# Performance work log

Hardware: AMD Instinct MI355X
Metric: run time of the kernel (lower is better)

The kernel has to match this reference:

```python
import math
import jax, jax.numpy as jnp
import numpy as np
from jax import lax

# ---- static config (mirrors RPN init + typical torchvision anchor setup) ----
IMG_H = IMG_W = 800
LEVELS = [(200, 200, 4, 32), (100, 100, 8, 64), (50, 50, 16, 128), (25, 25, 32, 256), (13, 13, 64, 512)]  # (h, w, stride, anchor_size)
RATIOS = (0.5, 1.0, 2.0)
COUNTS = tuple(h * w * len(RATIOS) for (h, w, _, _) in LEVELS)  # (120000,30000,7500,1875,507)
A_TOTAL = sum(COUNTS)  # 159882
PRE_NMS = 2000
POST_NMS = 1000
NMS_THRESH = 0.7
MIN_SIZE = 1e-3
BBOX_CLIP = math.log(1000.0 / 16)


def make_anchors():
    parts = []
    for (h, w, stride, size) in LEVELS:
        ws = np.array([size * np.sqrt(1.0 / r) for r in RATIOS], np.float32)  # [3]
        hs = np.array([size * np.sqrt(r) for r in RATIOS], np.float32)
        sx = (np.arange(w, dtype=np.float32) + 0.5) * stride
        sy = (np.arange(h, dtype=np.float32) + 0.5) * stride
        cy, cx = np.meshgrid(sy, sx, indexing='ij')
        cx = cx.reshape(-1, 1)
        cy = cy.reshape(-1, 1)
        a = np.stack([cx - ws / 2, cy - hs / 2, cx + ws / 2, cy + hs / 2], axis=-1)  # [HW,3,4]
        parts.append(a.reshape(-1, 4))
    return np.concatenate(parts, 0).astype(np.float32)


def setup_inputs() -> dict:
    key = jax.random.key(0)
    k1, k2 = jax.random.split(key)
    scores = jax.random.normal(k1, (1, A_TOTAL), dtype=jnp.float32)
    deltas = jax.random.normal(k2, (A_TOTAL, 4), dtype=jnp.float32) * 0.5
    anchors = jnp.asarray(make_anchors())
    return {'scores': scores, 'deltas': deltas, 'anchors': anchors}


def _pairwise_iou(b):
    area = (b[:, 2] - b[:, 0]) * (b[:, 3] - b[:, 1])  # [K]
    lt = jnp.maximum(b[:, None, :2], b[None, :, :2])   # [K,K,2]
    rb = jnp.minimum(b[:, None, 2:], b[None, :, 2:])
    wh = jnp.maximum(rb - lt, 0.0)
    inter = wh[..., 0] * wh[..., 1]
    return inter / (area[:, None] + area[None, :] - inter)


def reference(scores, deltas, anchors):
    s_all = lax.stop_gradient(scores[0])  # original does cls.detach()
    # ---- box decode (torchvision-style) ----
    w = anchors[:, 2] - anchors[:, 0]
    h = anchors[:, 3] - anchors[:, 1]
    cx = anchors[:, 0] + 0.5 * w
    cy = anchors[:, 1] + 0.5 * h
    dx, dy = deltas[:, 0], deltas[:, 1]
    dw = jnp.minimum(deltas[:, 2], BBOX_CLIP)
    dh = jnp.minimum(deltas[:, 3], BBOX_CLIP)
    px = cx + dx * w
    py = cy + dy * h
    pw = jnp.exp(dw) * w
    ph = jnp.exp(dh) * h
    boxes = jnp.stack([px - 0.5 * pw, py - 0.5 * ph, px + 0.5 * pw, py + 0.5 * ph], axis=1)  # [A,4]
    # ---- per-level top-k over objectness ----
    idx_parts = []
    off = 0
    for c in COUNTS:
        k = min(PRE_NMS, c)
        _, ti = lax.top_k(lax.dynamic_slice_in_dim(s_all, off, c), k)
        idx_parts.append(ti + off)
        off += c
    top_idx = jnp.concatenate(idx_parts)  # [K=8382]
    K = top_idx.shape[0]
    s = s_all[top_idx]
    b = boxes[top_idx]
    # ---- clip to image + min-size validity (masked instead of compacted) ----
    b = jnp.stack([jnp.clip(b[:, 0], 0.0, IMG_W), jnp.clip(b[:, 1], 0.0, IMG_H),
                   jnp.clip(b[:, 2], 0.0, IMG_W), jnp.clip(b[:, 3], 0.0, IMG_H)], axis=1)
    valid = ((b[:, 2] - b[:, 0]) >= MIN_SIZE) & ((b[:, 3] - b[:, 1]) >= MIN_SIZE)
    # ---- per-level NMS offset; replicates original feature_mask[keep] indexing
    # (positional indexing into the full anchor-order level-id vector) ----
    fmask_full = np.concatenate([np.full(c, i, np.float32) for i, c in enumerate(COUNTS)])
    fmask = jnp.asarray(fmask_full[:K])
    box_max = jnp.max(jnp.where(valid[:, None], b, -jnp.inf))
    bn = b + (fmask * (box_max + 1.0))[:, None]
    # ---- greedy NMS on score-sorted candidates ----
    s_m = jnp.where(valid, s, -jnp.inf)
    order = jnp.argsort(-s_m)
    s_srt = s_m[order]
    b_srt = b[order]
    iou = _pairwise_iou(bn[order])  # [K,K] ~281MB
    ar = jnp.arange(K)

    def body(i, keep):
        sup = (iou[i] > NMS_THRESH) & (ar > i)
        return jnp.where(keep[i], keep & ~sup, keep)

    keep = lax.fori_loop(0, K, body, s_srt > -jnp.inf)
    final = jnp.where(keep, s_srt, -jnp.inf)
    out_s, oidx = lax.top_k(final, POST_NMS)  # top post_nms kept, score order; -inf pads
    out_b = b_srt[oidx]
    return out_b, out_s
```

## Files before the change

kernel.cpp:

```cpp
#include <hip/hip_runtime.h>
#include <math.h>

typedef unsigned int u32;
typedef unsigned long long u64;
typedef unsigned char u8;

#define K_TOT 8382
#define NCH 131
#define CAP 1024
#define GCAP 32768
#define IMGSZ 800.0f

__device__ __constant__ int LOFF[5] = {0, 120000, 150000, 157500, 159375};
__device__ __constant__ int LCNT[5] = {120000, 30000, 7500, 1875, 507};
__device__ __constant__ int KSEL[5] = {2000, 2000, 2000, 1875, 507};
__device__ __constant__ int SELB[5] = {0, 2000, 4000, 6000, 7875};
__device__ __constant__ int HBS[4] = {0, 118, 148, 156};
__device__ __constant__ int GBS[6] = {0, 118, 148, 156, 158, 159};

static __device__ __forceinline__ u32 fkey(float x) {
    u32 u = __float_as_uint(x);
    u32 m = (u32)(((int)u) >> 31) | 0x80000000u;
    return u ^ m;
}

static __device__ __forceinline__ int lvl_of(int s) {
    return (s < 2000) ? 0 : (s < 4000) ? 1 : (s < 6000) ? 2 : (s < 7875) ? 3 : 4;
}

static __device__ __forceinline__ u32 rdl32(u32 v, int j) {
    return (u32)__builtin_amdgcn_readlane((int)v, j);
}
static __device__ __forceinline__ u64 rdlane64(u64 v, int j) {
    u32 lo = (u32)__builtin_amdgcn_readlane((int)(u32)v, j);
    u32 hi = (u32)__builtin_amdgcn_readlane((int)(u32)(v >> 32), j);
    return ((u64)hi << 32) | (u64)lo;
}

static __device__ __forceinline__ u32 wor32(u32 x) {
    x |= (u32)__builtin_amdgcn_update_dpp(0, (int)x, 0x111, 0xf, 0xf, true);
    x |= (u32)__builtin_amdgcn_update_dpp(0, (int)x, 0x112, 0xf, 0xf, true);
    x |= (u32)__builtin_amdgcn_update_dpp(0, (int)x, 0x114, 0xf, 0xf, true);
    x |= (u32)__builtin_amdgcn_update_dpp(0, (int)x, 0x118, 0xf, 0xf, true);
    x |= (u32)__builtin_amdgcn_update_dpp(0, (int)x, 0x142, 0xa, 0xf, true);
    x |= (u32)__builtin_amdgcn_update_dpp(0, (int)x, 0x143, 0xc, 0xf, true);
    return x;
}

static __device__ __forceinline__ void thresh_scan(const u32* hist, u32* scanbuf, int m,
                                                   u32 need, u32* sv, int t) {
    for (int i = t; i < m; i += 1024) scanbuf[i] = hist[m - 1 - i];
    __syncthreads();
    for (int ofs = 1; ofs < m; ofs <<= 1) {
        int i0 = t, i1 = t + 1024;
        u32 a0 = 0, a1 = 0;
        if (i0 < m && i0 >= ofs) a0 = scanbuf[i0 - ofs];
        if (i1 < m && i1 >= ofs) a1 = scanbuf[i1 - ofs];
        __syncthreads();
        if (i0 < m && i0 >= ofs) scanbuf[i0] += a0;
        if (i1 < m && i1 >= ofs) scanbuf[i1] += a1;
        __syncthreads();
    }
    for (int i = t; i < m; i += 1024) {
        u32 inc = scanbuf[i];
        u32 exc = i ? scanbuf[i - 1] : 0;
        if (inc >= need && exc < need) { sv[0] = (u32)(m - 1 - i); sv[1] = need - exc; }
    }
    __syncthreads();
}

__global__ __launch_bounds__(1024) void k_hist(const float* __restrict__ scores,
                                               u32* __restrict__ hist3) {
    __shared__ u32 lh[2048];
    int t = threadIdx.x;
    lh[t] = 0; lh[t + 1024] = 0;
    __syncthreads();
    int b = blockIdx.x;
    int l = (b < HBS[1]) ? 0 : (b < HBS[2]) ? 1 : 2;
    int i = (b - HBS[l]) * 1024 + t;
    if (i < LCNT[l]) atomicAdd(&lh[fkey(scores[LOFF[l] + i]) >> 21], 1u);
    __syncthreads();
    u32* h = hist3 + l * 2048;
    if (lh[t]) atomicAdd(&h[t], lh[t]);
    if (lh[t + 1024]) atomicAdd(&h[t + 1024], lh[t + 1024]);
}

__global__ __launch_bounds__(1024) void k_thresh(const u32* __restrict__ hist3,
                                                 u32* __restrict__ tinfo) {
    __shared__ u32 scanbuf[2048];
    __shared__ u32 sv[2];
    int l = blockIdx.x;
    int t = threadIdx.x;
    thresh_scan(hist3 + l * 2048, scanbuf, 2048, (u32)KSEL[l], sv, t);
    if (t == 0) { tinfo[l * 2] = sv[0]; tinfo[l * 2 + 1] = sv[1]; }
}

__global__ __launch_bounds__(1024) void k_gather(const float* __restrict__ scores,
                                                 const u32* __restrict__ tinfo,
                                                 u32* __restrict__ sel, u32* __restrict__ cgt,
                                                 u32* __restrict__ gcnt, u32* __restrict__ gidx,
                                                 u32* __restrict__ gkey) {
    int b = blockIdx.x;
    int l = (b < GBS[1]) ? 0 : (b < GBS[2]) ? 1 : (b < GBS[3]) ? 2 : (b < GBS[4]) ? 3 : 4;
    int i = (b - GBS[l]) * 1024 + threadIdx.x;
    if (i >= LCNT[l]) return;
    int off = LOFF[l], sb = SELB[l];
    if (l >= 3) { sel[sb + i] = (u32)(off + i); return; }
    u32 ky = fkey(scores[off + i]);
    u32 b1 = tinfo[l * 2];
    u32 top = ky >> 21;
    if (top > b1) {
        u32 p = atomicAdd(&cgt[l], 1u);
        sel[sb + p] = (u32)(off + i);
    } else if (top == b1) {
        u32 e = atomicAdd(&gcnt[l], 1u);
        if (e < GCAP) { gidx[l * GCAP + e] = (u32)i; gkey[l * GCAP + e] = ky; }
    }
}

__global__ __launch_bounds__(1024) void k_final(const u32* __restrict__ gidx,
                                                const u32* __restrict__ gkey,
                                                const u32* __restrict__ gcnt,
                                                const u32* __restrict__ tinfo,
                                                u32* __restrict__ sel) {
    __shared__ u32 hist[2048];
    __shared__ u32 scanbuf[2048];
    __shared__ u32 eqbuf[1024];
    __shared__ u32 sv[2];
    __shared__ u32 c2, ceq;
    int l = blockIdx.x;
    int t = threadIdx.x;
    int k = KSEL[l], sb = SELB[l], off = LOFF[l];
    u32 m = gcnt[l]; if (m > GCAP) m = GCAP;
    u32 b1 = tinfo[l * 2];
    u32 need = tinfo[l * 2 + 1];
    const u32* kb = gkey + l * GCAP;
    const u32* ib = gidx + l * GCAP;
    hist[t] = 0; hist[t + 1024] = 0; __syncthreads();
    for (u32 e = t; e < m; e += 1024) atomicAdd(&hist[(kb[e] >> 10) & 2047u], 1u);
    __syncthreads();
    thresh_scan(hist, scanbuf, 2048, need, sv, t);
    u32 b2 = sv[0], need2 = sv[1];
    __syncthreads();
    hist[t] = 0; __syncthreads();
    for (u32 e = t; e < m; e += 1024) {
        u32 ky = kb[e];
        if (((ky >> 10) & 2047u) == b2) atomicAdd(&hist[ky & 1023u], 1u);
    }
    __syncthreads();
    thresh_scan(hist, scanbuf, 1024, need2, sv, t);
    u32 T = (b1 << 21) | (b2 << 10) | sv[0];
    u32 take = sv[1];
    if (t == 0) { c2 = 0; ceq = 0; }
    __syncthreads();
    u32 nGTbin = need - take;
    u32 base2 = (u32)sb + (u32)k - need;
    for (u32 e = t; e < m; e += 1024) {
        u32 ky = kb[e];
        if (ky > T) { u32 p = atomicAdd(&c2, 1u); sel[base2 + p] = (u32)off + ib[e]; }
        else if (ky == T) { u32 q = atomicAdd(&ceq, 1u); if (q < 1024) eqbuf[q] = ib[e]; }
    }
    __syncthreads();
    if (t == 0) {
        int n = (ceq > 1024u) ? 1024 : (int)ceq;
        for (int a = 1; a < n; ++a) {
            u32 v = eqbuf[a]; int bq = a - 1;
            while (bq >= 0 && eqbuf[bq] > v) { eqbuf[bq + 1] = eqbuf[bq]; --bq; }
            eqbuf[bq + 1] = v;
        }
        for (u32 q = 0; q < take; ++q) sel[base2 + nGTbin + q] = (u32)off + eqbuf[q];
    }
}

__global__ void k_decode(const float* __restrict__ scores, const float4* __restrict__ deltas,
                         const float4* __restrict__ anchors, const u32* __restrict__ sel,
                         float4* __restrict__ candB, float* __restrict__ candS,
                         u32* __restrict__ candV, u32* __restrict__ candA) {
    int s = blockIdx.x * 256 + threadIdx.x;
    if (s >= K_TOT) return;
    u32 a = sel[s];
    float4 an = anchors[a];
    float4 dl = deltas[a];
    float sc = scores[a];
    float w = __fsub_rn(an.z, an.x), h = __fsub_rn(an.w, an.y);
    float cx = __fadd_rn(an.x, __fmul_rn(0.5f, w));
    float cy = __fadd_rn(an.y, __fmul_rn(0.5f, h));
    const float CLIPV = (float)4.1351665567423563;
    float dw = fminf(dl.z, CLIPV);
    float dh = fminf(dl.w, CLIPV);
    float px = __fadd_rn(cx, __fmul_rn(dl.x, w));
    float py = __fadd_rn(cy, __fmul_rn(dl.y, h));
    float pw = __fmul_rn((float)exp((double)dw), w);
    float ph = __fmul_rn((float)exp((double)dh), h);
    float x1 = __fsub_rn(px, __fmul_rn(0.5f, pw));
    float y1 = __fsub_rn(py, __fmul_rn(0.5f, ph));
    float x2 = __fadd_rn(px, __fmul_rn(0.5f, pw));
    float y2 = __fadd_rn(py, __fmul_rn(0.5f, ph));
    x1 = fminf(fmaxf(x1, 0.0f), IMGSZ);
    y1 = fminf(fmaxf(y1, 0.0f), IMGSZ);
    x2 = fminf(fmaxf(x2, 0.0f), IMGSZ);
    y2 = fminf(fmaxf(y2, 0.0f), IMGSZ);
    bool valid = (__fsub_rn(x2, x1) >= 0.001f) && (__fsub_rn(y2, y1) >= 0.001f);
    candB[s] = make_float4(x1, y1, x2, y2);
    candS[s] = sc;
    candV[s] = valid ? 1u : 0u;
    candA[s] = a;
}

__global__ __launch_bounds__(256) void k_rank_lvl(const float* __restrict__ candS,
                                                  const u32* __restrict__ candA,
                                                  u32* __restrict__ Praw) {
    __shared__ u64 tile[256];
    int l = blockIdx.z;
    int cnt = KSEL[l], base = SELB[l];
    int tx = blockIdx.x * 256;
    int ty = blockIdx.y * 256;
    if (tx >= cnt || ty >= cnt) return;
    int t = threadIdx.x;
    u64 Aj = ~0ull;
    if (tx + t < cnt) {
        int j = base + tx + t;
        Aj = ((u64)(~fkey(candS[j])) << 32) | (u64)candA[j];
    }
    tile[t] = Aj;
    __syncthreads();
    int si = ty + t;
    if (si >= cnt) return;
    int s = base + si;
    u64 A = ((u64)(~fkey(candS[s])) << 32) | (u64)candA[s];
    int r = 0;
#pragma unroll 8
    for (int q = 0; q < 256; ++q) r += (tile[q] < A);
    if (r) atomicAdd(&Praw[s], (u32)r);
}

__global__ __launch_bounds__(256) void k_rank_glob(const float* __restrict__ candS,
                                                   const u32* __restrict__ candV,
                                                   const u32* __restrict__ Praw,
                                                   u32* __restrict__ rank) {
    __shared__ u64 colB[256];
    int t = threadIdx.x;
    int cj = blockIdx.x * 256 + t;
    u64 B = ~0ull;
    if (cj < K_TOT) {
        u32 smk = candV[cj] ? fkey(candS[cj]) : 0x007FFFFFu;
        u32 Pj = (u32)SELB[lvl_of(cj)] + Praw[cj];
        B = ((u64)(~smk) << 32) | (u64)Pj;
    }
    colB[t] = B;
    __syncthreads();
    int s = blockIdx.y * 256 + t;
    if (s >= K_TOT) return;
    u32 smk = candV[s] ? fkey(candS[s]) : 0x007FFFFFu;
    u32 Ps = (u32)SELB[lvl_of(s)] + Praw[s];
    u64 myB = ((u64)(~smk) << 32) | (u64)Ps;
    int cnt = 0;
#pragma unroll 8
    for (int j = 0; j < 256; ++j) cnt += (colB[j] < myB);
    if (cnt) atomicAdd(&rank[s], (u32)cnt);
}

__global__ void k_scatter(const float4* __restrict__ candB, const float* __restrict__ candS,
                          const u32* __restrict__ candV, const u32* __restrict__ rank,
                          float4* __restrict__ sB, float* __restrict__ sArea,
                          float* __restrict__ sS, u32* __restrict__ sV) {
    int s = blockIdx.x * 256 + threadIdx.x;
    if (s >= K_TOT) return;
    u32 r = rank[s];
    float4 b = candB[s];
    float area = __fmul_rn(__fsub_rn(b.z, b.x), __fsub_rn(b.w, b.y));
    sB[r] = b; sArea[r] = area; sS[r] = candS[s]; sV[r] = candV[s];
}

__global__ __launch_bounds__(256) void k_mask(const float4* __restrict__ sB,
                                              const float* __restrict__ sArea,
                                              const u32* __restrict__ sV,
                                              u64* __restrict__ vwords,
                                              u64* __restrict__ diag, u32* __restrict__ ecnt,
                                              ulonglong2* __restrict__ epack,
                                              u64* __restrict__ dmask) {
    __shared__ float4 cb[64];
    __shared__ float ca[64];
    int wd = blockIdx.x;
    int t = threadIdx.x;
    if (t < 64) {
        int j = wd * 64 + t;
        if (j < K_TOT) { cb[t] = sB[j]; ca[t] = sArea[j]; }
        else { cb[t] = make_float4(0.f, 0.f, 0.f, 0.f); ca[t] = 0.f; }
    }
    __syncthreads();
    int i = blockIdx.y * 256 + t;
    if (i >= K_TOT) return;
    int dwr = i >> 6;
    if (wd < dwr) return;
    float4 bi = sB[i];
    float ai = sArea[i];
    u64 bits = 0;
    int jbase = wd * 64;
    for (int j2 = 0; j2 < 64; ++j2) {
        int j = jbase + j2;
        if (j > i && j < K_TOT) {
            float4 bj = cb[j2];
            float ltx = fmaxf(bi.x, bj.x), lty = fmaxf(bi.y, bj.y);
            float rbx = fminf(bi.z, bj.z), rby = fminf(bi.w, bj.w);
            float wx = fmaxf(__fsub_rn(rbx, ltx), 0.0f);
            float wy = fmaxf(__fsub_rn(rby, lty), 0.0f);
            float inter = __fmul_rn(wx, wy);
            if (inter > 0.0f) {
                float uni = __fsub_rn(__fadd_rn(ai, ca[j2]), inter);
                float iou = inter / uni;
                if (iou > 0.7f) bits |= (1ull << j2);
            }
        }
    }
    if (wd == dwr) {
        diag[i] = bits;
        u64 vb = __ballot(sV[i] != 0u);
        u64 db = __ballot(bits != 0ull);
        if ((i & 63) == 0) { vwords[wd] = vb; dmask[wd] = db; }
    } else if (bits != 0ull) {
        u32 p = atomicAdd(&ecnt[wd], 1u);
        if (p < CAP) epack[wd * CAP + p] = make_ulonglong2((u64)i, bits);
    }
}

__global__ __launch_bounds__(1024) void k_scan(const u64* __restrict__ diag,
                                               const u64* __restrict__ vwords,
                                               const u32* __restrict__ ecnt,
                                               const ulonglong2* __restrict__ tpack,
                                               const u64* __restrict__ dmask,
                                               const float4* __restrict__ sB,
                                               const float* __restrict__ sS,
                                               float* __restrict__ out) {
    __shared__ u64 sKeepArr[NCH];
    __shared__ u32 pc[NCH + 1];
    __shared__ u32 sProg;
    int t = threadIdx.x;
    int w = t >> 6, lane = t & 63;
    if (t == 0) sProg = 0;
    __syncthreads();
    if (w < 4) {
        for (int c = w; c < NCH; c += 4) {
            ulonglong2 E1 = tpack[(size_t)c * CAP + lane];
            ulonglong2 E2 = tpack[(size_t)c * CAP + 64 + lane];
            u64 Dc = diag[c * 64 + lane];
            u64 vw = vwords[c];
            u64 dmw = dmask[c];
            u32 cnt = ecnt[c]; if (cnt > CAP) cnt = CAP;
            u32 s1 = (u32)E1.x, s2 = (u32)E2.x;
            u32 sch1 = s1 >> 6, sch2 = s2 >> 6;
            u64 mbits = 0;
            bool done1 = ((u32)lane >= cnt);
            bool done2 = ((u32)(lane + 64) >= cnt);
            if (c > 0) {
                for (;;) {
                    u32 p = __hip_atomic_load(&sProg, __ATOMIC_ACQUIRE, __HIP_MEMORY_SCOPE_WORKGROUP);
                    if ((u32)c > p + 2u) { __builtin_amdgcn_s_sleep(2); continue; }
                    if (!done1 && sch1 < p) {
                        if ((sKeepArr[sch1] >> (s1 & 63u)) & 1ull) mbits |= E1.y;
                        done1 = true;
                    }
                    if (!done2 && sch2 < p) {
                        if ((sKeepArr[sch2] >> (s2 & 63u)) & 1ull) mbits |= E2.y;
                        done2 = true;
                    }
                    if (p >= (u32)c) break;
                }
            }
            u64 inc = 0;
            if (cnt) {
                if (cnt > 128u) {
                    for (u32 e = 128u + (u32)lane; e < cnt; e += 64u) {
                        ulonglong2 Et = tpack[(size_t)c * CAP + e];
                        u32 si = (u32)Et.x;
                        if ((sKeepArr[si >> 6] >> (si & 63u)) & 1ull) mbits |= Et.y;
                    }
                }
                u32 lo = wor32((u32)mbits);
                u32 hi = wor32((u32)(mbits >> 32));
                inc = ((u64)rdl32(hi, 63) << 32) | (u64)rdl32(lo, 63);
            }
            u64 alive = vw & ~inc;
            if (dmw) {
                u64 dm = dmw & alive;
                while (dm) {
                    int j = __builtin_ctzll(dm);
                    dm &= dm - 1;
                    if ((alive >> j) & 1ull) {
                        alive &= ~rdlane64(Dc, j);
                        dm &= alive;
                    }
                }
            }
            if (lane == 0) {
                sKeepArr[c] = alive;
                __hip_atomic_store(&sProg, (u32)(c + 1), __ATOMIC_RELEASE, __HIP_MEMORY_SCOPE_WORKGROUP);
            }
        }
    }
    __syncthreads();
    if (t < NCH) pc[t + 1] = (u32)__popcll(sKeepArr[t]);
    if (t == 0) pc[0] = 0;
    __syncthreads();
    for (int ofs = 1; ofs < NCH; ofs <<= 1) {
        int i = t + 1;
        u32 v = 0;
        bool p = (t < NCH) && (i - ofs >= 1);
        if (p) v = pc[i - ofs];
        __syncthreads();
        if (p) pc[i] += v;
        __syncthreads();
    }
    u32 nk = pc[NCH];
    for (int i = t; i < K_TOT; i += 1024) {
        int wi = i >> 6, b = i & 63;
        u64 kw = sKeepArr[wi];
        u32 kb = pc[wi] + (u32)__popcll(kw & ((1ull << b) - 1ull));
        bool kp = (kw >> b) & 1ull;
        if (kp) {
            if (kb < 1000u) {
                float4 bx = sB[i];
                out[kb * 4 + 0] = bx.x; out[kb * 4 + 1] = bx.y;
                out[kb * 4 + 2] = bx.z; out[kb * 4 + 3] = bx.w;
                out[4000 + kb] = sS[i];
            }
        } else {
            u32 q = (u32)i - kb;
            u32 slot = nk + q;
            if (slot < 1000u) {
                float4 bx = sB[i];
                out[slot * 4 + 0] = bx.x; out[slot * 4 + 1] = bx.y;
                out[slot * 4 + 2] = bx.z; out[slot * 4 + 3] = bx.w;
                out[4000 + slot] = -INFINITY;
            }
        }
    }
}

static constexpr size_t al256(size_t x) { return (x + 255) & ~(size_t)255; }
static constexpr size_t KB4 = (size_t)K_TOT * 4;
static constexpr size_t KB16 = (size_t)K_TOT * 16;
static constexpr size_t O_RANK = 0;
static constexpr size_t O_PRAW = al256(O_RANK + KB4);
static constexpr size_t O_ECNT = al256(O_PRAW + KB4);
static constexpr size_t O_HIST = al256(O_ECNT + (size_t)NCH * 4);
static constexpr size_t O_CGT = al256(O_HIST + (size_t)3 * 2048 * 4);
static constexpr size_t O_GCNT = al256(O_CGT + 3 * 4);
static constexpr size_t MEMSET_BYTES = al256(O_GCNT + 3 * 4);
static constexpr size_t O_TINFO = MEMSET_BYTES;
static constexpr size_t O_SEL = al256(O_TINFO + 6 * 4);
static constexpr size_t O_GIDX = al256(O_SEL + KB4);
static constexpr size_t O_GKEY = al256(O_GIDX + (size_t)3 * GCAP * 4);
static constexpr size_t O_CANDB = al256(O_GKEY + (size_t)3 * GCAP * 4);
static constexpr size_t O_CANDS = al256(O_CANDB + KB16);
static constexpr size_t O_CANDV = al256(O_CANDS + KB4);
static constexpr size_t O_CANDA = al256(O_CANDV + KB4);
static constexpr size_t O_SB = al256(O_CANDA + KB4);
static constexpr size_t O_SAREA = al256(O_SB + KB16);
static constexpr size_t O_SS = al256(O_SAREA + KB4);
static constexpr size_t O_SV = al256(O_SS + KB4);
static constexpr size_t O_VW = al256(O_SV + KB4);
static constexpr size_t O_DMASK = al256(O_VW + (size_t)NCH * 8);
static constexpr size_t O_DIAG = al256(O_DMASK + (size_t)NCH * 8);
static constexpr size_t O_EPACK = al256(O_DIAG + (size_t)(NCH * 64) * 8);

extern "C" void kernel_launch(void* const* d_in, const int* in_sizes, int n_in,
                              void* d_out, int out_size, void* d_ws, size_t ws_size,
                              hipStream_t stream) {
    const float* scores = (const float*)d_in[0];
    const float4* deltas = (const float4*)d_in[1];
    const float4* anchors = (const float4*)d_in[2];
    float* out = (float*)d_out;
    char* ws = (char*)d_ws;

    u32* rank = (u32*)(ws + O_RANK);
    u32* Praw = (u32*)(ws + O_PRAW);
    u32* ecnt = (u32*)(ws + O_ECNT);
    u32* hist3 = (u32*)(ws + O_HIST);
    u32* cgt = (u32*)(ws + O_CGT);
    u32* gcnt = (u32*)(ws + O_GCNT);
    u32* tinfo = (u32*)(ws + O_TINFO);
    u32* sel = (u32*)(ws + O_SEL);
    u32* gidx = (u32*)(ws + O_GIDX);
    u32* gkey = (u32*)(ws + O_GKEY);
    float4* candB = (float4*)(ws + O_CANDB);
    float* candS = (float*)(ws + O_CANDS);
    u32* candV = (u32*)(ws + O_CANDV);
    u32* candA = (u32*)(ws + O_CANDA);
    float4* sB = (float4*)(ws + O_SB);
    float* sArea = (float*)(ws + O_SAREA);
    float* sS = (float*)(ws + O_SS);
    u32* sV = (u32*)(ws + O_SV);
    u64* vwords = (u64*)(ws + O_VW);
    u64* dmask = (u64*)(ws + O_DMASK);
    u64* diag = (u64*)(ws + O_DIAG);
    ulonglong2* epack = (ulonglong2*)(ws + O_EPACK);

    hipMemsetAsync(ws, 0, MEMSET_BYTES, stream);

    const int NBLK = (K_TOT + 255) / 256;
    k_hist<<<156, 1024, 0, stream>>>(scores, hist3);
    k_thresh<<<3, 1024, 0, stream>>>(hist3, tinfo);
    k_gather<<<159, 1024, 0, stream>>>(scores, tinfo, sel, cgt, gcnt, gidx, gkey);
    k_final<<<3, 1024, 0, stream>>>(gidx, gkey, gcnt, tinfo, sel);
    k_decode<<<NBLK, 256, 0, stream>>>(scores, deltas, anchors, sel, candB, candS, candV, candA);
    k_rank_lvl<<<dim3(8, 8, 5), 256, 0, stream>>>(candS, candA, Praw);
    k_rank_glob<<<dim3(NBLK, NBLK), 256, 0, stream>>>(candS, candV, Praw, rank);
    k_scatter<<<NBLK, 256, 0, stream>>>(candB, candS, candV, rank, sB, sArea, sS, sV);
    k_mask<<<dim3(NCH, NBLK), 256, 0, stream>>>(sB, sArea, sV, vwords, diag, ecnt, epack, dmask);
    k_scan<<<1, 1024, 0, stream>>>(diag, vwords, ecnt, epack, dmask, sB, sS, out);
}
```

Baseline: 209.2 us.

## Batch four NMS chunks per wave in serial scan to cut handoffs

The serial NMS keep-mask scan now has each wave resolve a super-chunk of four consecutive 64-box chunks. Dependencies inside a super-chunk are forwarded in registers, so the number of cross-wave shared-memory progress handoffs drops by about four times. All tpack, diag and mask loads for the four chunks are issued up front to hide their latency. In exchange, a wave now waits for the previous super-chunk to finish completely rather than consuming partial progress. The block shrinks from 1024 to 512 threads, which halves the parallelism of the output-writing loop.

```diff
diff --git a/kernel.cpp b/kernel.cpp
--- a/kernel.cpp
+++ b/kernel.cpp
@@ -7,6 +7,8 @@
 
 #define K_TOT 8382
 #define NCH 131
+#define SC 4
+#define NSC ((NCH + SC - 1) / SC)
 #define CAP 1024
 #define GCAP 32768
 #define IMGSZ 800.0f
@@ -324,77 +326,172 @@
     }
 }
 
-__global__ __launch_bounds__(1024) void k_scan(const u64* __restrict__ diag,
-                                               const u64* __restrict__ vwords,
-                                               const u32* __restrict__ ecnt,
-                                               const ulonglong2* __restrict__ tpack,
-                                               const u64* __restrict__ dmask,
-                                               const float4* __restrict__ sB,
-                                               const float* __restrict__ sS,
-                                               float* __restrict__ out) {
-    __shared__ u64 sKeepArr[NCH];
+__global__ __launch_bounds__(512) void k_scan(const u64* __restrict__ diag,
+                                              const u64* __restrict__ vwords,
+                                              const u32* __restrict__ ecnt,
+                                              const ulonglong2* __restrict__ tpack,
+                                              const u64* __restrict__ dmask,
+                                              const float4* __restrict__ sB,
+                                              const float* __restrict__ sS,
+                                              float* __restrict__ out) {
+    __shared__ u64 sKeepArr[NSC * SC];
     __shared__ u32 pc[NCH + 1];
     __shared__ u32 sProg;
     int t = threadIdx.x;
     int w = t >> 6, lane = t & 63;
     if (t == 0) sProg = 0;
+    if (t < NSC * SC) sKeepArr[t] = 0;
     __syncthreads();
     if (w < 4) {
-        for (int c = w; c < NCH; c += 4) {
-            ulonglong2 E1 = tpack[(size_t)c * CAP + lane];
-            ulonglong2 E2 = tpack[(size_t)c * CAP + 64 + lane];
-            u64 Dc = diag[c * 64 + lane];
-            u64 vw = vwords[c];
-            u64 dmw = dmask[c];
-            u32 cnt = ecnt[c]; if (cnt > CAP) cnt = CAP;
-            u32 s1 = (u32)E1.x, s2 = (u32)E2.x;
-            u32 sch1 = s1 >> 6, sch2 = s2 >> 6;
-            u64 mbits = 0;
-            bool done1 = ((u32)lane >= cnt);
-            bool done2 = ((u32)(lane + 64) >= cnt);
-            if (c > 0) {
+        for (int C = w; C < NSC; C += 4) {
+            int w0 = C * SC;
+            int t0 = w0, t1 = w0 + 1, t2 = w0 + 2, t3 = w0 + 3;
+            bool x1v = t1 < NCH, x2v = t2 < NCH, x3v = t3 < NCH;
+            int q1 = x1v ? t1 : 0, q2 = x2v ? t2 : 0, q3 = x3v ? t3 : 0;
+            u32 c0 = ecnt[t0], c1 = x1v ? ecnt[q1] : 0, c2 = x2v ? ecnt[q2] : 0, c3 = x3v ? ecnt[q3] : 0;
+            if (c0 > CAP) c0 = CAP;
+            if (c1 > CAP) c1 = CAP;
+            if (c2 > CAP) c2 = CAP;
+            if (c3 > CAP) c3 = CAP;
+            u64 vw0 = vwords[t0];
+            u64 vw1 = x1v ? vwords[q1] : 0;
+            u64 vw2 = x2v ? vwords[q2] : 0;
+            u64 vw3 = x3v ? vwords[q3] : 0;
+            u64 dmw0 = dmask[t0];
+            u64 dmw1 = x1v ? dmask[q1] : 0;
+            u64 dmw2 = x2v ? dmask[q2] : 0;
+            u64 dmw3 = x3v ? dmask[q3] : 0;
+            u64 D0 = diag[t0 * 64 + lane];
+            u64 D1 = diag[q1 * 64 + lane];
+            u64 D2 = diag[q2 * 64 + lane];
+            u64 D3 = diag[q3 * 64 + lane];
+            ulonglong2 E00 = tpack[(size_t)t0 * CAP + lane];
+            ulonglong2 E01 = tpack[(size_t)t0 * CAP + 64 + lane];
+            ulonglong2 E10 = tpack[(size_t)q1 * CAP + lane];
+            ulonglong2 E11 = tpack[(size_t)q1 * CAP + 64 + lane];
+            ulonglong2 E20 = tpack[(size_t)q2 * CAP + lane];
+            ulonglong2 E21 = tpack[(size_t)q2 * CAP + 64 + lane];
+            ulonglong2 E30 = tpack[(size_t)q3 * CAP + lane];
+            ulonglong2 E31 = tpack[(size_t)q3 * CAP + 64 + lane];
+            u32 s00 = (u32)E00.x, s01 = (u32)E01.x, s10 = (u32)E10.x, s11 = (u32)E11.x;
+            u32 s20 = (u32)E20.x, s21 = (u32)E21.x, s30 = (u32)E30.x, s31 = (u32)E31.x;
+            u32 h00 = s00 >> 6, h01 = s01 >> 6, h10 = s10 >> 6, h11 = s11 >> 6;
+            u32 h20 = s20 >> 6, h21 = s21 >> 6, h30 = s30 >> 6, h31 = s31 >> 6;
+            if (C > 0) {
                 for (;;) {
                     u32 p = __hip_atomic_load(&sProg, __ATOMIC_ACQUIRE, __HIP_MEMORY_SCOPE_WORKGROUP);
-                    if ((u32)c > p + 2u) { __builtin_amdgcn_s_sleep(2); continue; }
-                    if (!done1 && sch1 < p) {
-                        if ((sKeepArr[sch1] >> (s1 & 63u)) & 1ull) mbits |= E1.y;
-                        done1 = true;
-                    }
-                    if (!done2 && sch2 < p) {
-                        if ((sKeepArr[sch2] >> (s2 & 63u)) & 1ull) mbits |= E2.y;
-                        done2 = true;
-                    }
-                    if (p >= (u32)c) break;
-                }
-            }
-            u64 inc = 0;
-            if (cnt) {
-                if (cnt > 128u) {
-                    for (u32 e = 128u + (u32)lane; e < cnt; e += 64u) {
-                        ulonglong2 Et = tpack[(size_t)c * CAP + e];
-                        u32 si = (u32)Et.x;
-                        if ((sKeepArr[si >> 6] >> (si & 63u)) & 1ull) mbits |= Et.y;
-                    }
-                }
-                u32 lo = wor32((u32)mbits);
-                u32 hi = wor32((u32)(mbits >> 32));
-                inc = ((u64)rdl32(hi, 63) << 32) | (u64)rdl32(lo, 63);
-            }
-            u64 alive = vw & ~inc;
-            if (dmw) {
-                u64 dm = dmw & alive;
-                while (dm) {
-                    int j = __builtin_ctzll(dm);
-                    dm &= dm - 1;
-                    if ((alive >> j) & 1ull) {
-                        alive &= ~rdlane64(Dc, j);
-                        dm &= alive;
-                    }
+                    if (p >= (u32)C) break;
+                    if ((u32)C > p + 1u) __builtin_amdgcn_s_sleep(2);
+                }
+            }
+            u64 K00 = sKeepArr[h00 < (u32)NCH ? h00 : 0u];
+            u64 K01 = sKeepArr[h01 < (u32)NCH ? h01 : 0u];
+            u64 K10 = sKeepArr[h10 < (u32)NCH ? h10 : 0u];
+            u64 K11 = sKeepArr[h11 < (u32)NCH ? h11 : 0u];
+            u64 K20 = sKeepArr[h20 < (u32)NCH ? h20 : 0u];
+            u64 K21 = sKeepArr[h21 < (u32)NCH ? h21 : 0u];
+            u64 K30 = sKeepArr[h30 < (u32)NCH ? h30 : 0u];
+            u64 K31 = sKeepArr[h31 < (u32)NCH ? h31 : 0u];
+            u64 m = 0;
+            if ((u32)lane < c0 && ((K00 >> (s00 & 63u)) & 1ull)) m = E00.y;
+            if ((u32)(lane + 64) < c0 && ((K01 >> (s01 & 63u)) & 1ull)) m |= E01.y;
+            if (c0 > 128u) {
+                for (u32 e = 128u + (u32)lane; e < c0; e += 64u) {
+                    ulonglong2 Et = tpack[(size_t)t0 * CAP + e];
+                    u32 si = (u32)Et.x;
+                    if ((sKeepArr[si >> 6] >> (si & 63u)) & 1ull) m |= Et.y;
+                }
+            }
+            u32 lo = wor32((u32)m), hi = wor32((u32)(m >> 32));
+            u64 inc = ((u64)rdl32(hi, 63) << 32) | (u64)rdl32(lo, 63);
+            u64 alive0 = vw0 & ~inc;
+            if (dmw0) {
+                u64 d = dmw0 & alive0;
+                while (d) {
+                    int j = __builtin_ctzll(d);
+                    d &= d - 1;
+                    if ((alive0 >> j) & 1ull) { alive0 &= ~rdlane64(D0, j); d &= alive0; }
+                }
+            }
+            u64 kwA = (h10 == (u32)t0) ? alive0 : K10;
+            u64 kwB = (h11 == (u32)t0) ? alive0 : K11;
+            m = 0;
+            if ((u32)lane < c1 && ((kwA >> (s10 & 63u)) & 1ull)) m = E10.y;
+            if ((u32)(lane + 64) < c1 && ((kwB >> (s11 & 63u)) & 1ull)) m |= E11.y;
+            if (c1 > 128u) {
+                for (u32 e = 128u + (u32)lane; e < c1; e += 64u) {
+                    ulonglong2 Et = tpack[(size_t)q1 * CAP + e];
+                    u32 si = (u32)Et.x; u32 hh = si >> 6;
+                    u64 kw = (hh == (u32)t0) ? alive0 : sKeepArr[hh];
+                    if ((kw >> (si & 63u)) & 1ull) m |= Et.y;
+                }
+            }
+            lo = wor32((u32)m); hi = wor32((u32)(m >> 32));
+            inc = ((u64)rdl32(hi, 63) << 32) | (u64)rdl32(lo, 63);
+            u64 alive1 = vw1 & ~inc;
+            if (dmw1) {
+                u64 d = dmw1 & alive1;
+                while (d) {
+                    int j = __builtin_ctzll(d);
+                    d &= d - 1;
+                    if ((alive1 >> j) & 1ull) { alive1 &= ~rdlane64(D1, j); d &= alive1; }
+                }
+            }
+            kwA = (h20 == (u32)t0) ? alive0 : (h20 == (u32)t1) ? alive1 : K20;
+            kwB = (h21 == (u32)t0) ? alive0 : (h21 == (u32)t1) ? alive1 : K21;
+            m = 0;
+            if ((u32)lane < c2 && ((kwA >> (s20 & 63u)) & 1ull)) m = E20.y;
+            if ((u32)(lane + 64) < c2 && ((kwB >> (s21 & 63u)) & 1ull)) m |= E21.y;
+            if (c2 > 128u) {
+                for (u32 e = 128u + (u32)lane; e < c2; e += 64u) {
+                    ulonglong2 Et = tpack[(size_t)q2 * CAP + e];
+                    u32 si = (u32)Et.x; u32 hh = si >> 6;
+                    u64 kw = (hh == (u32)t0) ? alive0 : (hh == (u32)t1) ? alive1 : sKeepArr[hh];
+                    if ((kw >> (si & 63u)) & 1ull) m |= Et.y;
+                }
+            }
+            lo = wor32((u32)m); hi = wor32((u32)(m >> 32));
+            inc = ((u64)rdl32(hi, 63) << 32) | (u64)rdl32(lo, 63);
+            u64 alive2 = vw2 & ~inc;
+            if (dmw2) {
+                u64 d = dmw2 & alive2;
+                while (d) {
+                    int j = __builtin_ctzll(d);
+                    d &= d - 1;
+                    if ((alive2 >> j) & 1ull) { alive2 &= ~rdlane64(D2, j); d &= alive2; }
+                }
+            }
+            kwA = (h30 == (u32)t0) ? alive0 : (h30 == (u32)t1) ? alive1 : (h30 == (u32)t2) ? alive2 : K30;
+            kwB = (h31 == (u32)t0) ? alive0 : (h31 == (u32)t1) ? alive1 : (h31 == (u32)t2) ? alive2 : K31;
+            m = 0;
+            if ((u32)lane < c3 && ((kwA >> (s30 & 63u)) & 1ull)) m = E30.y;
+            if ((u32)(lane + 64) < c3 && ((kwB >> (s31 & 63u)) & 1ull)) m |= E31.y;
+            if (c3 > 128u) {
+                for (u32 e = 128u + (u32)lane; e < c3; e += 64u) {
+                    ulonglong2 Et = tpack[(size_t)q3 * CAP + e];
+                    u32 si = (u32)Et.x; u32 hh = si >> 6;
+                    u64 kw = (hh == (u32)t0) ? alive0 : (hh == (u32)t1) ? alive1
+                           : (hh == (u32)t2) ? alive2 : sKeepArr[hh];
+                    if ((kw >> (si & 63u)) & 1ull) m |= Et.y;
+                }
+            }
+            lo = wor32((u32)m); hi = wor32((u32)(m >> 32));
+            inc = ((u64)rdl32(hi, 63) << 32) | (u64)rdl32(lo, 63);
+            u64 alive3 = vw3 & ~inc;
+            if (dmw3) {
+                u64 d = dmw3 & alive3;
+                while (d) {
+                    int j = __builtin_ctzll(d);
+                    d &= d - 1;
+                    if ((alive3 >> j) & 1ull) { alive3 &= ~rdlane64(D3, j); d &= alive3; }
                 }
             }
             if (lane == 0) {
-                sKeepArr[c] = alive;
-                __hip_atomic_store(&sProg, (u32)(c + 1), __ATOMIC_RELEASE, __HIP_MEMORY_SCOPE_WORKGROUP);
+                sKeepArr[t0] = alive0;
+                sKeepArr[t1] = alive1;
+                sKeepArr[t2] = alive2;
+                sKeepArr[t3] = alive3;
+                __hip_atomic_store(&sProg, (u32)(C + 1), __ATOMIC_RELEASE, __HIP_MEMORY_SCOPE_WORKGROUP);
             }
         }
     }
@@ -412,7 +509,7 @@
         __syncthreads();
     }
     u32 nk = pc[NCH];
-    for (int i = t; i < K_TOT; i += 1024) {
+    for (int i = t; i < K_TOT; i += 512) {
         int wi = i >> 6, b = i & 63;
         u64 kw = sKeepArr[wi];
         u32 kb = pc[wi] + (u32)__popcll(kw & ((1ull << b) - 1ull));
@@ -508,5 +605,5 @@
     k_rank_glob<<<dim3(NBLK, NBLK), 256, 0, stream>>>(candS, candV, Praw, rank);
     k_scatter<<<NBLK, 256, 0, stream>>>(candB, candS, candV, rank, sB, sArea, sS, sV);
     k_mask<<<dim3(NCH, NBLK), 256, 0, stream>>>(sB, sArea, sV, vwords, diag, ecnt, epack, dmask);
-    k_scan<<<1, 1024, 0, stream>>>(diag, vwords, ecnt, epack, dmask, sB, sS, out);
-}
+    k_scan<<<1, 512, 0, stream>>>(diag, vwords, ecnt, epack, dmask, sB, sS, out);
+}
```

After: 194.6 us. 7.0% less time.
